# Kernel optimization log

Measured on AMD Instinct MI355X. Metric: run time of the kernel, lower is better.

The kernel has to match this reference:

```python
import jax, jax.numpy as jnp
import numpy as np

NEG_RATIO = 3.0           # negative_ratio
FALLBACK_NEG = 0.0        # fallback_negative_num
EPS = 1e-6                # eps
LOG_CLAMP = -100.0        # torch BCELoss clamps log to -100


def setup_inputs() -> dict:
    key = jax.random.key(0)
    k1, k2, k3 = jax.random.split(key, 3)
    shape = (32, 640, 640)  # [B, H, W] DBNet-style shrink maps
    # probabilities strictly inside (0,1)
    pred = jax.random.uniform(k1, shape, jnp.float32, 1e-4, 1.0 - 1e-4)
    gt = (jax.random.uniform(k2, shape) < 0.05).astype(jnp.float32)
    mask = (jax.random.uniform(k3, shape) < 0.9).astype(jnp.float32)
    return {"pred": pred, "gt": gt, "mask": mask}


def reference(pred, gt, mask):
    positive = gt * mask
    negative = (1.0 - gt) * mask
    # torch uses int(sum()); masks are binary so sums are integral, floor is exact
    pos_count = jnp.floor(positive.sum())
    neg_total = jnp.floor(negative.sum())
    neg_count = jnp.where(
        pos_count == 0,
        jnp.minimum(neg_total, FALLBACK_NEG),
        jnp.minimum(neg_total, jnp.floor(pos_count * NEG_RATIO)),
    )

    # BCE with torch's log clamp at -100
    log_p = jnp.maximum(jnp.log(pred), LOG_CLAMP)
    log_1mp = jnp.maximum(jnp.log1p(-pred), LOG_CLAMP)
    loss = -(gt * log_p + (1.0 - gt) * log_1mp)

    positive_sum = (loss * positive).sum()

    # hard-negative mining: take the top `neg_count` negative losses.
    # neg_count is data-dependent, so sort descending and mask by rank
    # (jit-compatible, same math as torch.topk(...).sum()).
    neg_loss = (loss * negative).reshape(-1)
    neg_sorted = -jnp.sort(-neg_loss)  # descending
    ranks = jnp.arange(neg_sorted.shape[0], dtype=jnp.float32)
    negative_sum = jnp.where(ranks < neg_count, neg_sorted, 0.0).sum()

    return (positive_sum + negative_sum) / (pos_count + neg_count + EPS)
```

## Files before the change

### kernel.cpp

```cpp
#include <hip/hip_runtime.h>
#include <math.h>


#define NBINS1 4096
#define K1_BLOCKS 1024

struct Ctrl {
  unsigned long long pos_cnt;
  unsigned long long neg_cnt;
  unsigned long long k;
  double pos_sum;
  unsigned B;
  unsigned k_rem;
};

#define LN2F 0.69314718055994530942f

__device__ __forceinline__ double bin_mid(unsigned b) {
  return (double)__uint_as_float((b << 19) | 0x40000u);
}

__device__ __forceinline__ void proc1(float p, float g, float m,
                                      unsigned& pc, unsigned& nc,
                                      double& psum, unsigned* __restrict__ hc) {
  bool gpos = (g != 0.0f);
  bool valid = (m != 0.0f);
  bool ispos = valid && gpos;
  bool isneg = valid && !gpos;
  float x = gpos ? p : 1.0f - p;
  float loss = -fmaxf(__log2f(x) * LN2F, -100.0f);
  pc += ispos ? 1u : 0u;
  nc += isneg ? 1u : 0u;
  psum += ispos ? (double)loss : 0.0;
  if (isneg) atomicAdd(&hc[__float_as_uint(loss) >> 19], 1u);
}

extern "C" __global__ void __launch_bounds__(256, 4)
k1_hist(const float* __restrict__ pred, const float* __restrict__ gt,
        const float* __restrict__ mask, unsigned* __restrict__ hist1,
        Ctrl* __restrict__ ctrl, int n4, int n) {
  __shared__ unsigned h[2][NBINS1];
  for (int i = threadIdx.x; i < 2 * NBINS1; i += blockDim.x)
    ((unsigned*)h)[i] = 0u;
  __syncthreads();

  int wv = threadIdx.x >> 6, ln = threadIdx.x & 63;
  unsigned* hc = h[wv & 1];

  unsigned pc = 0, nc = 0;
  double psum = 0.0;
  const float4* p4 = (const float4*)pred;
  const float4* g4 = (const float4*)gt;
  const float4* m4 = (const float4*)mask;
  int gtid = blockIdx.x * blockDim.x + threadIdx.x;
  int S = gridDim.x * blockDim.x;

  int i = gtid;
  for (; i + 3 * S < n4; i += 4 * S) {
    float4 pv0 = p4[i];
    float4 pv1 = p4[i + S];
    float4 pv2 = p4[i + 2 * S];
    float4 pv3 = p4[i + 3 * S];
    float4 gv0 = g4[i];
    float4 gv1 = g4[i + S];
    float4 gv2 = g4[i + 2 * S];
    float4 gv3 = g4[i + 3 * S];
    float4 mv0 = m4[i];
    float4 mv1 = m4[i + S];
    float4 mv2 = m4[i + 2 * S];
    float4 mv3 = m4[i + 3 * S];

    proc1(pv0.x, gv0.x, mv0.x, pc, nc, psum, hc);
    proc1(pv0.y, gv0.y, mv0.y, pc, nc, psum, hc);
    proc1(pv0.z, gv0.z, mv0.z, pc, nc, psum, hc);
    proc1(pv0.w, gv0.w, mv0.w, pc, nc, psum, hc);
    proc1(pv1.x, gv1.x, mv1.x, pc, nc, psum, hc);
    proc1(pv1.y, gv1.y, mv1.y, pc, nc, psum, hc);
    proc1(pv1.z, gv1.z, mv1.z, pc, nc, psum, hc);
    proc1(pv1.w, gv1.w, mv1.w, pc, nc, psum, hc);
    proc1(pv2.x, gv2.x, mv2.x, pc, nc, psum, hc);
    proc1(pv2.y, gv2.y, mv2.y, pc, nc, psum, hc);
    proc1(pv2.z, gv2.z, mv2.z, pc, nc, psum, hc);
    proc1(pv2.w, gv2.w, mv2.w, pc, nc, psum, hc);
    proc1(pv3.x, gv3.x, mv3.x, pc, nc, psum, hc);
    proc1(pv3.y, gv3.y, mv3.y, pc, nc, psum, hc);
    proc1(pv3.z, gv3.z, mv3.z, pc, nc, psum, hc);
    proc1(pv3.w, gv3.w, mv3.w, pc, nc, psum, hc);
  }
  for (; i < n4; i += S) {
    float4 pv = p4[i], gv = g4[i], mv = m4[i];
    proc1(pv.x, gv.x, mv.x, pc, nc, psum, hc);
    proc1(pv.y, gv.y, mv.y, pc, nc, psum, hc);
    proc1(pv.z, gv.z, mv.z, pc, nc, psum, hc);
    proc1(pv.w, gv.w, mv.w, pc, nc, psum, hc);
  }
  for (int t = n4 * 4 + gtid; t < n; t += S) {
    proc1(pred[t], gt[t], mask[t], pc, nc, psum, hc);
  }

  unsigned long long pcl = pc, ncl = nc;
  for (int off = 32; off > 0; off >>= 1) {
    pcl += __shfl_down(pcl, off);
    ncl += __shfl_down(ncl, off);
    psum += __shfl_down(psum, off);
  }
  __shared__ unsigned long long spc[4], snc[4];
  __shared__ double sps[4];
  if (ln == 0) { spc[wv] = pcl; snc[wv] = ncl; sps[wv] = psum; }
  __syncthreads();
  if (threadIdx.x == 0) {
    unsigned long long tp = 0, tn = 0; double ts = 0.0;
    for (int w = 0; w < 4; w++) { tp += spc[w]; tn += snc[w]; ts += sps[w]; }
    atomicAdd(&ctrl->pos_cnt, tp);
    atomicAdd(&ctrl->neg_cnt, tn);
    unsafeAtomicAdd(&ctrl->pos_sum, ts);
  }
  for (int b = threadIdx.x; b < NBINS1; b += blockDim.x) {
    unsigned c = h[0][b] + h[1][b];
    if (c) atomicAdd(&hist1[b], c);
  }
}

extern "C" __global__ void __launch_bounds__(256)
k5_final(const unsigned* __restrict__ hist1, Ctrl* __restrict__ ctrl,
         float* __restrict__ out) {
  const int T = 256, CH = NBINS1 / T;
  __shared__ unsigned long long sarr[T];
  __shared__ unsigned long long sk;
  __shared__ unsigned sB, skrem;
  __shared__ double sred[4];
  int t = threadIdx.x;
  int wv = t >> 6, ln = t & 63;

  unsigned cnt[CH];
  unsigned long long tot = 0;
  for (int j = 0; j < CH; j++) { cnt[j] = hist1[t * CH + j]; tot += cnt[j]; }
  sarr[t] = tot;
  if (t == 0) {
    sB = 0xFFFFFFFFu; skrem = 0u;
    unsigned long long pos = ctrl->pos_cnt, negtot = ctrl->neg_cnt;
    unsigned long long k = 0;
    if (pos > 0) {
      k = pos * 3ull;
      if (k > negtot) k = negtot;
    }
    ctrl->k = k;
    sk = k;
  }
  __syncthreads();
  for (int off = 1; off < T; off <<= 1) {
    unsigned long long v = (t + off < T) ? sarr[t + off] : 0ull;
    __syncthreads();
    sarr[t] += v;
    __syncthreads();
  }
  unsigned long long k = sk;
  if (k > 0) {
    unsigned long long above = sarr[t] - tot;
    if (above < k && sarr[t] >= k) {
      unsigned long long cum = above;
      for (int j = CH - 1; j >= 0; j--) {
        if (cum + (unsigned long long)cnt[j] >= k) {
          sB = (unsigned)(t * CH + j);
          skrem = (unsigned)(k - cum);
          break;
        }
        cum += cnt[j];
      }
    }
  }
  __syncthreads();
  unsigned B = sB;

  double s = 0.0;
  if (B != 0xFFFFFFFFu) {
    for (int j = 0; j < CH; j++) {
      unsigned bi = (unsigned)(t * CH + j);
      if (bi > B && cnt[j]) s += (double)cnt[j] * bin_mid(bi);
    }
  }
  for (int off = 32; off > 0; off >>= 1) s += __shfl_down(s, off);
  if (ln == 0) sred[wv] = s;
  __syncthreads();
  if (t == 0) {
    double neg_sum = sred[0] + sred[1] + sred[2] + sred[3];
    if (skrem > 0 && B != 0xFFFFFFFFu)
      neg_sum += (double)skrem * bin_mid(B);
    double denom = (double)ctrl->pos_cnt + (double)k + 1e-6;
    out[0] = (float)((ctrl->pos_sum + neg_sum) / denom);
  }
}

extern "C" void kernel_launch(void* const* d_in, const int* in_sizes, int n_in,
                              void* d_out, int out_size, void* d_ws, size_t ws_size,
                              hipStream_t stream) {
  const float* pred = (const float*)d_in[0];
  const float* gt   = (const float*)d_in[1];
  const float* mask = (const float*)d_in[2];
  float* out = (float*)d_out;
  int n = in_sizes[0];
  int n4 = n / 4;
  char* ws = (char*)d_ws;

  const size_t HIST1_OFF = 256;
  const size_t ZERO_BYTES = HIST1_OFF + NBINS1 * sizeof(unsigned);

  Ctrl* ctrl = (Ctrl*)ws;
  unsigned* hist1 = (unsigned*)(ws + HIST1_OFF);

  hipMemsetAsync(d_ws, 0, ZERO_BYTES, stream);
  k1_hist<<<K1_BLOCKS, 256, 0, stream>>>(pred, gt, mask, hist1, ctrl, n4, n);
  k5_final<<<1, 256, 0, stream>>>(hist1, ctrl, out);
}
```

Measured before the change: 189.2 us.

## Use single shared histogram per block and double grid size with higher occupancy

Collapses the two per-block LDS histogram copies into one, halving shared memory per block. This lets launch bounds target 8 blocks per CU, and the grid grows from 1024 to 2048 blocks to give more latency hiding on the memory-bound pass. The trade-off is more LDS atomic contention, since all four waves now share one histogram. It also doubles the number of blocks that flush their histograms into the global one with atomics.

```diff
diff --git a/kernel.cpp b/kernel.cpp
--- a/kernel.cpp
+++ b/kernel.cpp
@@ -3,7 +3,7 @@
 
 
 #define NBINS1 4096
-#define K1_BLOCKS 1024
+#define K1_BLOCKS 2048
 
 struct Ctrl {
   unsigned long long pos_cnt;
@@ -35,17 +35,15 @@
   if (isneg) atomicAdd(&hc[__float_as_uint(loss) >> 19], 1u);
 }
 
-extern "C" __global__ void __launch_bounds__(256, 4)
+extern "C" __global__ void __launch_bounds__(256, 8)
 k1_hist(const float* __restrict__ pred, const float* __restrict__ gt,
         const float* __restrict__ mask, unsigned* __restrict__ hist1,
         Ctrl* __restrict__ ctrl, int n4, int n) {
-  __shared__ unsigned h[2][NBINS1];
-  for (int i = threadIdx.x; i < 2 * NBINS1; i += blockDim.x)
-    ((unsigned*)h)[i] = 0u;
+  __shared__ unsigned h[NBINS1];
+  for (int i = threadIdx.x; i < NBINS1; i += blockDim.x) h[i] = 0u;
   __syncthreads();
 
   int wv = threadIdx.x >> 6, ln = threadIdx.x & 63;
-  unsigned* hc = h[wv & 1];
 
   unsigned pc = 0, nc = 0;
   double psum = 0.0;
@@ -70,32 +68,32 @@
     float4 mv2 = m4[i + 2 * S];
     float4 mv3 = m4[i + 3 * S];
 
-    proc1(pv0.x, gv0.x, mv0.x, pc, nc, psum, hc);
-    proc1(pv0.y, gv0.y, mv0.y, pc, nc, psum, hc);
-    proc1(pv0.z, gv0.z, mv0.z, pc, nc, psum, hc);
-    proc1(pv0.w, gv0.w, mv0.w, pc, nc, psum, hc);
-    proc1(pv1.x, gv1.x, mv1.x, pc, nc, psum, hc);
-    proc1(pv1.y, gv1.y, mv1.y, pc, nc, psum, hc);
-    proc1(pv1.z, gv1.z, mv1.z, pc, nc, psum, hc);
-    proc1(pv1.w, gv1.w, mv1.w, pc, nc, psum, hc);
-    proc1(pv2.x, gv2.x, mv2.x, pc, nc, psum, hc);
-    proc1(pv2.y, gv2.y, mv2.y, pc, nc, psum, hc);
-    proc1(pv2.z, gv2.z, mv2.z, pc, nc, psum, hc);
-    proc1(pv2.w, gv2.w, mv2.w, pc, nc, psum, hc);
-    proc1(pv3.x, gv3.x, mv3.x, pc, nc, psum, hc);
-    proc1(pv3.y, gv3.y, mv3.y, pc, nc, psum, hc);
-    proc1(pv3.z, gv3.z, mv3.z, pc, nc, psum, hc);
-    proc1(pv3.w, gv3.w, mv3.w, pc, nc, psum, hc);
+    proc1(pv0.x, gv0.x, mv0.x, pc, nc, psum, h);
+    proc1(pv0.y, gv0.y, mv0.y, pc, nc, psum, h);
+    proc1(pv0.z, gv0.z, mv0.z, pc, nc, psum, h);
+    proc1(pv0.w, gv0.w, mv0.w, pc, nc, psum, h);
+    proc1(pv1.x, gv1.x, mv1.x, pc, nc, psum, h);
+    proc1(pv1.y, gv1.y, mv1.y, pc, nc, psum, h);
+    proc1(pv1.z, gv1.z, mv1.z, pc, nc, psum, h);
+    proc1(pv1.w, gv1.w, mv1.w, pc, nc, psum, h);
+    proc1(pv2.x, gv2.x, mv2.x, pc, nc, psum, h);
+    proc1(pv2.y, gv2.y, mv2.y, pc, nc, psum, h);
+    proc1(pv2.z, gv2.z, mv2.z, pc, nc, psum, h);
+    proc1(pv2.w, gv2.w, mv2.w, pc, nc, psum, h);
+    proc1(pv3.x, gv3.x, mv3.x, pc, nc, psum, h);
+    proc1(pv3.y, gv3.y, mv3.y, pc, nc, psum, h);
+    proc1(pv3.z, gv3.z, mv3.z, pc, nc, psum, h);
+    proc1(pv3.w, gv3.w, mv3.w, pc, nc, psum, h);
   }
   for (; i < n4; i += S) {
     float4 pv = p4[i], gv = g4[i], mv = m4[i];
-    proc1(pv.x, gv.x, mv.x, pc, nc, psum, hc);
-    proc1(pv.y, gv.y, mv.y, pc, nc, psum, hc);
-    proc1(pv.z, gv.z, mv.z, pc, nc, psum, hc);
-    proc1(pv.w, gv.w, mv.w, pc, nc, psum, hc);
+    proc1(pv.x, gv.x, mv.x, pc, nc, psum, h);
+    proc1(pv.y, gv.y, mv.y, pc, nc, psum, h);
+    proc1(pv.z, gv.z, mv.z, pc, nc, psum, h);
+    proc1(pv.w, gv.w, mv.w, pc, nc, psum, h);
   }
   for (int t = n4 * 4 + gtid; t < n; t += S) {
-    proc1(pred[t], gt[t], mask[t], pc, nc, psum, hc);
+    proc1(pred[t], gt[t], mask[t], pc, nc, psum, h);
   }
 
   unsigned long long pcl = pc, ncl = nc;
@@ -116,7 +114,7 @@
     unsafeAtomicAdd(&ctrl->pos_sum, ts);
   }
   for (int b = threadIdx.x; b < NBINS1; b += blockDim.x) {
-    unsigned c = h[0][b] + h[1][b];
+    unsigned c = h[b];
     if (c) atomicAdd(&hist1[b], c);
   }
 }
```

Result: slower. 224.0 us (+18.4%).
